# Kernel tuning notes

Hardware: AMD Instinct MI355X
Metric: run time of the kernel (lower is better)

## Reference

```python
import math
import jax, jax.numpy as jnp
import numpy as np

N_HEAD = 16
LORA_SCALE = 16.0 / 8.0  # lora_alpha / r


def lora_linear(x, W, b, A, B):
    # y = x @ W^T + b + scale * (x @ A^T) @ B^T
    base = jnp.einsum('btc,oc->bto', x, W) + b
    low = jnp.einsum('btc,rc->btr', x, A)
    return base + LORA_SCALE * jnp.einsum('btr,or->bto', low, B)


def setup_inputs() -> dict:
    key = jax.random.key(0)
    ks = jax.random.split(key, 8)
    B, T, C = 2, 2048, 1024
    r = 8
    s = 0.02
    return {
        'x': jax.random.normal(ks[0], (B, T, C), jnp.float32),
        'W_attn': jax.random.normal(ks[1], (3 * C, C), jnp.float32) * s,
        'b_attn': jnp.zeros((3 * C,), jnp.float32),
        'A_attn': jax.random.normal(ks[2], (r, C), jnp.float32) * s,
        'B_attn': jax.random.normal(ks[3], (3 * C, r), jnp.float32) * s,
        'W_proj': jax.random.normal(ks[4], (C, C), jnp.float32) * s,
        'b_proj': jnp.zeros((C,), jnp.float32),
        'A_proj': jax.random.normal(ks[5], (r, C), jnp.float32) * s,
        'B_proj': jax.random.normal(ks[6], (C, r), jnp.float32) * s,
    }


def reference(x, W_attn, b_attn, A_attn, B_attn, W_proj, b_proj, A_proj, B_proj):
    B, T, C = x.shape
    H = N_HEAD
    hd = C // H
    qkv = lora_linear(x, W_attn, b_attn, A_attn, B_attn)  # [B,T,3C]
    q, k, v = jnp.split(qkv, 3, axis=2)
    # [B,H,T,hd]
    q = q.reshape(B, T, H, hd).transpose(0, 2, 1, 3)
    k = k.reshape(B, T, H, hd).transpose(0, 2, 1, 3)
    v = v.reshape(B, T, H, hd).transpose(0, 2, 1, 3)
    att = jnp.einsum('bhqd,bhkd->bhqk', q, k) * (1.0 / math.sqrt(hd))
    causal = jnp.tril(jnp.ones((T, T), bool))
    att = jnp.where(causal, att, -jnp.inf)
    att = jax.nn.softmax(att, axis=-1)
    out = jnp.einsum('bhqk,bhkd->bhqd', att, v)
    out = out.transpose(0, 2, 1, 3).reshape(B, T, C)
    return lora_linear(out, W_proj, b_proj, A_proj, B_proj)
```

## Files before the change

kernel.cpp:

```cpp
#include <hip/hip_runtime.h>
#include <hip/hip_bf16.h>
#include <stdint.h>

typedef __bf16 bf16_t;
typedef __bf16 bf16x8 __attribute__((ext_vector_type(8)));
typedef __bf16 bf16x4 __attribute__((ext_vector_type(4)));
typedef __bf16 bf16x2 __attribute__((ext_vector_type(2)));
typedef float f32x4 __attribute__((ext_vector_type(4)));
typedef float f32x16 __attribute__((ext_vector_type(16)));
typedef uint32_t u32;
typedef uint32_t u32x4 __attribute__((ext_vector_type(4)));

typedef __attribute__((address_space(1))) void as1void;
typedef __attribute__((address_space(3))) void as3void;

#define LOG2E 1.44269504088896340736f
#define QSCALE 0.18033688011112042f

__device__ __forceinline__ void gll16(const void* g, void* l) {
  __builtin_amdgcn_global_load_lds((as1void*)g, (as3void*)l, 16, 0, 0);
}

__device__ __forceinline__ u32 pack2(float a, float b) {
  bf16x2 t = {(bf16_t)a, (bf16_t)b};
  return __builtin_bit_cast(u32, t);
}

__global__ void prep_all(const float* __restrict__ W_attn, const float* __restrict__ B_attn,
                         const float* __restrict__ A_attn, const float* __restrict__ W_proj,
                         const float* __restrict__ B_proj, const float* __restrict__ A_proj,
                         const float4* __restrict__ x,
                         bf16_t* __restrict__ WaE, bf16_t* __restrict__ WpE,
                         bf16x4* __restrict__ Xb) {
  int bid = blockIdx.x;
  if (bid < 16384) {
    int idx = bid * 256 + threadIdx.x;
    const float *W, *Bm, *Am;
    bf16_t* dst;
    if (idx < 3145728) {
      W = W_attn; Bm = B_attn; Am = A_attn; dst = WaE;
    } else {
      idx -= 3145728;
      W = W_proj; Bm = B_proj; Am = A_proj; dst = WpE;
    }
    int o = idx >> 10, c = idx & 1023;
    float acc = W[idx];
#pragma unroll
    for (int r = 0; r < 8; ++r)
      acc += 2.0f * Bm[o * 8 + r] * Am[r * 1024 + c];
    dst[idx] = (bf16_t)acc;
  } else {
    int i = (bid - 16384) * 256 + threadIdx.x;
    float4 v = x[i];
    bf16x4 o = {(bf16_t)v.x, (bf16_t)v.y, (bf16_t)v.z, (bf16_t)v.w};
    Xb[i] = o;
  }
}

template <bool QKV>
__global__ __launch_bounds__(256, 3) void gemm_bt(
    const bf16_t* __restrict__ A, const bf16_t* __restrict__ Bt,
    const float* __restrict__ bias,
    bf16_t* __restrict__ Qb, bf16_t* __restrict__ Kb, bf16_t* __restrict__ Vb,
    float* __restrict__ Out) {
  __shared__ bf16_t Als[128][64];
  __shared__ bf16_t Bls[128][64];
  const int m0 = blockIdx.x * 128;
  const int n0 = blockIdx.y * 128;
  const int tid = threadIdx.x;
  const int lane = tid & 63;
  const int w = tid >> 6;
  const int wm = w >> 1, wn = w & 1;
  const int lr = lane & 15, g = lane >> 4;
  const int sw = (lane & 7) << 3;
  const int srow = lane >> 3;
  const int soff = ((lane & 7) ^ srow) * 8;

  f32x4 acc[4][4] = {};

  for (int k0 = 0; k0 < 1024; k0 += 64) {
#pragma unroll
    for (int c = 0; c < 4; ++c) {
      int r = w * 32 + c * 8 + srow;
      gll16(A + (size_t)(m0 + r) * 1024 + k0 + soff, &Als[w * 32 + c * 8][0]);
      gll16(Bt + (size_t)(n0 + r) * 1024 + k0 + soff, &Bls[w * 32 + c * 8][0]);
    }
    __syncthreads();
#pragma unroll
    for (int ks = 0; ks < 2; ++ks) {
      bf16x8 af[4], bfv[4];
#pragma unroll
      for (int i = 0; i < 4; ++i)
        af[i] = *(const bf16x8*)&Als[wm * 64 + i * 16 + lr][(ks * 32 + g * 8) ^ sw];
#pragma unroll
      for (int j = 0; j < 4; ++j)
        bfv[j] = *(const bf16x8*)&Bls[wn * 64 + j * 16 + lr][(ks * 32 + g * 8) ^ sw];
#pragma unroll
      for (int i = 0; i < 4; ++i)
#pragma unroll
        for (int j = 0; j < 4; ++j)
          acc[i][j] = __builtin_amdgcn_mfma_f32_16x16x32_bf16(af[i], bfv[j], acc[i][j], 0, 0, 0);
    }
    __syncthreads();
  }

#pragma unroll
  for (int i = 0; i < 4; ++i) {
#pragma unroll
    for (int j = 0; j < 4; ++j) {
#pragma unroll
      for (int e = 0; e < 4; ++e) {
        int m = m0 + wm * 64 + i * 16 + g * 4 + e;
        int n = n0 + wn * 64 + j * 16 + lr;
        float v = acc[i][j][e] + bias[n];
        if (QKV) {
          int b = m >> 11, t = m & 2047;
          int which = n >> 10, hn = n & 1023;
          int h = hn >> 6, d = hn & 63;
          if (which == 0) v *= QSCALE;
          bf16_t* dst = (which == 0) ? Qb : (which == 1) ? Kb : Vb;
          dst[(((size_t)(b * 16 + h)) * 2048 + t) * 64 + d] = (bf16_t)v;
        } else {
          Out[(size_t)m * 1024 + n] = v;
        }
      }
    }
  }
}

__global__ __launch_bounds__(256, 3) void attn_fwd(
    const bf16_t* __restrict__ Qb, const bf16_t* __restrict__ Kb,
    const bf16_t* __restrict__ Vb, bf16_t* __restrict__ Ob) {
  __shared__ bf16_t Kls[128][64];
  __shared__ bf16_t Vt[2][64][128];

  int id = blockIdx.x;
  int xcd = id & 7, j = id >> 3;
  int lo = j & 31, hi2 = j >> 5;
  int bh = xcd * 4 + (lo & 3);
  int qb = hi2 ? 15 - (lo >> 2) : (lo >> 2);
  int b = bh >> 4, h = bh & 15;

  const int tid = threadIdx.x, lane = tid & 63, w = tid >> 6;
  const int q32 = lane & 31;
  const int hi = lane >> 5;
  const int ksw = (q32 & 7) << 3;
  const int vkey = (q32 >> 2) << 3;
  const bf16_t* Qp = Qb + (size_t)bh * 2048 * 64;
  const bf16_t* Kp = Kb + (size_t)bh * 2048 * 64;
  const bf16_t* Vp = Vb + (size_t)bh * 2048 * 64;

  const int q0 = qb * 128;
  const int qrow = q0 + w * 32 + q32;

  const int kbase = (tid >> 4) * 8;
  const int dbase = (tid & 15) * 4;
  const int wkey = ((tid & 15) & 7) << 3;
  const int ksr = lane >> 3;
  const int kso = ((lane & 7) ^ ksr) * 8;

  bf16x8 qf[4];
#pragma unroll
  for (int ds = 0; ds < 4; ++ds)
    qf[ds] = *(const bf16x8*)(Qp + (size_t)qrow * 64 + ds * 16 + hi * 8);

  float m_run = -3e38f, l_run = 0.f;
  f32x16 o_acc[2] = {};
  const int ktiles = qb + 1;

  {
#pragma unroll
    for (int c = 0; c < 4; ++c) {
      int rb = w * 32 + c * 8;
      gll16(Kp + (size_t)(rb + ksr) * 64 + kso, &Kls[rb][0]);
    }
    uint2 rowv[8];
#pragma unroll
    for (int r = 0; r < 8; ++r)
      rowv[r] = *(const uint2*)(Vp + (size_t)(kbase + r) * 64 + dbase);
#pragma unroll
    for (int dd = 0; dd < 4; ++dd) {
      u32 sel = (dd & 1) ? 0x07060302u : 0x05040100u;
      u32 a0 = (dd >> 1) ? rowv[0].y : rowv[0].x;
      u32 a1 = (dd >> 1) ? rowv[1].y : rowv[1].x;
      u32 a2 = (dd >> 1) ? rowv[2].y : rowv[2].x;
      u32 a3 = (dd >> 1) ? rowv[3].y : rowv[3].x;
      u32 a4 = (dd >> 1) ? rowv[4].y : rowv[4].x;
      u32 a5 = (dd >> 1) ? rowv[5].y : rowv[5].x;
      u32 a6 = (dd >> 1) ? rowv[6].y : rowv[6].x;
      u32 a7 = (dd >> 1) ? rowv[7].y : rowv[7].x;
      int4 val;
      val.x = __builtin_amdgcn_perm(a1, a0, sel);
      val.y = __builtin_amdgcn_perm(a3, a2, sel);
      val.z = __builtin_amdgcn_perm(a5, a4, sel);
      val.w = __builtin_amdgcn_perm(a7, a6, sel);
      *(int4*)&Vt[0][dbase + dd][kbase ^ wkey] = val;
    }
    __syncthreads();
  }

  int cb = 0;
  for (int kt = 0; kt < ktiles; ++kt) {
    const bool lastt = (kt == ktiles - 1);
    const int nfa = lastt ? (w + 1) : 4;
    const int nb = cb ^ 1;

    f32x16 s[4] = {};
    __builtin_amdgcn_s_setprio(1);
#pragma unroll
    for (int fa = 0; fa < 4; ++fa) {
      if (fa < nfa) {
#pragma unroll
        for (int ds = 0; ds < 4; ++ds) {
          bf16x8 kf = *(const bf16x8*)&Kls[fa * 32 + q32][(ds * 16 + hi * 8) ^ ksw];
          s[fa] = __builtin_amdgcn_mfma_f32_32x32x16_bf16(kf, qf[ds], s[fa], 0, 0, 0);
        }
      }
    }
    __builtin_amdgcn_s_setprio(0);
    __syncthreads();

    uint2 rowv[8];
    if (!lastt) {
      const int kn = (kt + 1) * 128;
#pragma unroll
      for (int c = 0; c < 4; ++c) {
        int rb = w * 32 + c * 8;
        gll16(Kp + (size_t)(kn + rb + ksr) * 64 + kso, &Kls[rb][0]);
      }
#pragma unroll
      for (int r = 0; r < 8; ++r)
        rowv[r] = *(const uint2*)(Vp + (size_t)(kn + kbase + r) * 64 + dbase);
    }

    float mloc = -3e38f;
#pragma unroll
    for (int fa = 0; fa < 4; ++fa) {
      if (fa < nfa) {
        if (lastt && fa == w) {
#pragma unroll
          for (int r = 0; r < 16; ++r) {
            int km = (r & 3) + 8 * (r >> 2) + 4 * hi;
            if (km > q32) s[fa][r] = -3e38f;
          }
        }
#pragma unroll
        for (int r = 0; r < 16; ++r) mloc = fmaxf(mloc, s[fa][r]);
      }
    }
    mloc = fmaxf(mloc, __shfl_xor(mloc, 32, 64));
    if (!__all(mloc <= m_run + 8.0f)) {
      float mnew = fmaxf(m_run, mloc);
      float rs = __builtin_amdgcn_exp2f(m_run - mnew);
      m_run = mnew;
      l_run *= rs;
      o_acc[0] *= rs;
      o_acc[1] *= rs;
    }

    if (!lastt) {
#pragma unroll
      for (int dd = 0; dd < 4; ++dd) {
        u32 sel = (dd & 1) ? 0x07060302u : 0x05040100u;
        u32 a0 = (dd >> 1) ? rowv[0].y : rowv[0].x;
        u32 a1 = (dd >> 1) ? rowv[1].y : rowv[1].x;
        u32 a2 = (dd >> 1) ? rowv[2].y : rowv[2].x;
        u32 a3 = (dd >> 1) ? rowv[3].y : rowv[3].x;
        u32 a4 = (dd >> 1) ? rowv[4].y : rowv[4].x;
        u32 a5 = (dd >> 1) ? rowv[5].y : rowv[5].x;
        u32 a6 = (dd >> 1) ? rowv[6].y : rowv[6].x;
        u32 a7 = (dd >> 1) ? rowv[7].y : rowv[7].x;
        int4 val;
        val.x = __builtin_amdgcn_perm(a1, a0, sel);
        val.y = __builtin_amdgcn_perm(a3, a2, sel);
        val.z = __builtin_amdgcn_perm(a5, a4, sel);
        val.w = __builtin_amdgcn_perm(a7, a6, sel);
        *(int4*)&Vt[nb][dbase + dd][kbase ^ wkey] = val;
      }
    }

    float lsum = 0.f;
#pragma unroll
    for (int fa = 0; fa < 4; ++fa) {
      if (fa < nfa) {
        float p[16];
#pragma unroll
        for (int r = 0; r < 16; ++r) {
          p[r] = __builtin_amdgcn_exp2f(s[fa][r] - m_run);
          lsum += p[r];
        }
        u32 x0 = pack2(p[0], p[1]),   x1 = pack2(p[2], p[3]);
        u32 x2 = pack2(p[4], p[5]),   x3 = pack2(p[6], p[7]);
        u32 y0 = pack2(p[8], p[9]),   y1 = pack2(p[10], p[11]);
        u32 y2 = pack2(p[12], p[13]), y3 = pack2(p[14], p[15]);
        u32 z0 = hi ? x0 : x2;
        u32 z1 = hi ? x1 : x3;
        u32 z2 = hi ? y0 : y2;
        u32 z3 = hi ? y1 : y3;
        z0 = (u32)__shfl_xor((int)z0, 32, 64);
        z1 = (u32)__shfl_xor((int)z1, 32, 64);
        z2 = (u32)__shfl_xor((int)z2, 32, 64);
        z3 = (u32)__shfl_xor((int)z3, 32, 64);
        u32x4 pw0 = hi ? (u32x4){z0, z1, x2, x3} : (u32x4){x0, x1, z0, z1};
        u32x4 pw1 = hi ? (u32x4){z2, z3, y2, y3} : (u32x4){y0, y1, z2, z3};
        bf16x8 P0 = __builtin_bit_cast(bf16x8, pw0);
        bf16x8 P1 = __builtin_bit_cast(bf16x8, pw1);
        __builtin_amdgcn_s_setprio(1);
#pragma unroll
        for (int db = 0; db < 2; ++db) {
          int d = db * 32 + q32;
          bf16x8 vf0 = *(const bf16x8*)&Vt[cb][d][(fa * 32 + hi * 8) ^ vkey];
          o_acc[db] = __builtin_amdgcn_mfma_f32_32x32x16_bf16(vf0, P0, o_acc[db], 0, 0, 0);
          bf16x8 vf1 = *(const bf16x8*)&Vt[cb][d][(fa * 32 + 16 + hi * 8) ^ vkey];
          o_acc[db] = __builtin_amdgcn_mfma_f32_32x32x16_bf16(vf1, P1, o_acc[db], 0, 0, 0);
        }
        __builtin_amdgcn_s_setprio(0);
      }
    }
    lsum += __shfl_xor(lsum, 32, 64);
    l_run += lsum;

    __syncthreads();
    cb = nb;
  }

  float inv = 1.0f / l_run;
  bf16_t* obase = Ob + ((size_t)(b * 2048 + qrow)) * 1024 + h * 64;
#pragma unroll
  for (int db = 0; db < 2; ++db) {
#pragma unroll
    for (int rg = 0; rg < 4; ++rg) {
      bf16x4 ov = {(bf16_t)(o_acc[db][rg * 4 + 0] * inv),
                   (bf16_t)(o_acc[db][rg * 4 + 1] * inv),
                   (bf16_t)(o_acc[db][rg * 4 + 2] * inv),
                   (bf16_t)(o_acc[db][rg * 4 + 3] * inv)};
      *(bf16x4*)(obase + db * 32 + rg * 8 + hi * 4) = ov;
    }
  }
}

extern "C" void kernel_launch(void* const* d_in, const int* in_sizes, int n_in,
                              void* d_out, int out_size, void* d_ws, size_t ws_size,
                              hipStream_t stream) {
  const float* x      = (const float*)d_in[0];
  const float* W_attn = (const float*)d_in[1];
  const float* b_attn = (const float*)d_in[2];
  const float* A_attn = (const float*)d_in[3];
  const float* B_attn = (const float*)d_in[4];
  const float* W_proj = (const float*)d_in[5];
  const float* b_proj = (const float*)d_in[6];
  const float* A_proj = (const float*)d_in[7];
  const float* B_proj = (const float*)d_in[8];
  float* out = (float*)d_out;

  char* ws = (char*)d_ws;
  bf16_t* WaE = (bf16_t*)(ws);
  bf16_t* WpE = (bf16_t*)(ws + 6291456);
  bf16_t* Xb  = (bf16_t*)(ws + 8388608);
  bf16_t* Qb  = (bf16_t*)(ws + 16777216);
  bf16_t* Kb  = (bf16_t*)(ws + 25165824);
  bf16_t* Vb  = (bf16_t*)(ws + 33554432);
  bf16_t* Ob  = (bf16_t*)(ws + 41943040);

  prep_all<<<20480, 256, 0, stream>>>(W_attn, B_attn, A_attn, W_proj, B_proj, A_proj,
                                      (const float4*)x, WaE, WpE, (bf16x4*)Xb);

  gemm_bt<true><<<dim3(32, 24), 256, 0, stream>>>(Xb, WaE, b_attn, Qb, Kb, Vb, nullptr);
  attn_fwd<<<512, 256, 0, stream>>>(Qb, Kb, Vb, Ob);
  gemm_bt<false><<<dim3(32, 8), 256, 0, stream>>>(Ob, WpE, b_proj, nullptr, nullptr, nullptr, out);
}
```

Baseline: 118.6 us.

## Split long causal query blocks across two workgroups and merge partial softmax results

Query blocks 8-15 now have their key range split into two halves, each handled by its own workgroup, which writes unnormalized partial outputs plus running max and sum to workspace. A new merge kernel combines them. Blocks are ordered by descending work through a constant table to balance load. K is also double-buffered in LDS so one barrier per tile is dropped, and the V-transpose swizzle changes. The cost is extra partial-output traffic, an extra kernel launch, lower occupancy (launch bounds 2), and reuse of the weight/X workspace regions for partials.

```diff
diff --git a/kernel.cpp b/kernel.cpp
--- a/kernel.cpp
+++ b/kernel.cpp
@@ -14,8 +14,11 @@
 typedef __attribute__((address_space(1))) void as1void;
 typedef __attribute__((address_space(3))) void as3void;
 
-#define LOG2E 1.44269504088896340736f
 #define QSCALE 0.18033688011112042f
+
+__constant__ unsigned char kOrder[24] = {7, 20, 22, 23, 6, 16, 18, 19, 21,
+                                         5, 12, 14, 15, 17, 4, 8, 10, 11, 13,
+                                         3, 9, 2, 1, 0};
 
 __device__ __forceinline__ void gll16(const void* g, void* l) {
   __builtin_amdgcn_global_load_lds((as1void*)g, (as3void*)l, 16, 0, 0);
@@ -128,24 +131,34 @@
   }
 }
 
-__global__ __launch_bounds__(256, 3) void attn_fwd(
+__global__ __launch_bounds__(256, 2) void attn_fwd(
     const bf16_t* __restrict__ Qb, const bf16_t* __restrict__ Kb,
-    const bf16_t* __restrict__ Vb, bf16_t* __restrict__ Ob) {
-  __shared__ bf16_t Kls[128][64];
+    const bf16_t* __restrict__ Vb, bf16_t* __restrict__ Ob,
+    bf16_t* __restrict__ Po, float* __restrict__ Pml) {
+  __shared__ bf16_t Kls[2][128][64];
   __shared__ bf16_t Vt[2][64][128];
 
   int id = blockIdx.x;
-  int xcd = id & 7, j = id >> 3;
-  int lo = j & 31, hi2 = j >> 5;
-  int bh = xcd * 4 + (lo & 3);
-  int qb = hi2 ? 15 - (lo >> 2) : (lo >> 2);
+  int xcd = id & 7, r = id >> 3;
+  int bh = xcd * 4 + (r & 3);
+  int j = kOrder[r >> 2];
+  int qb, kt0, kt1, part;
+  if (j < 8) {
+    qb = j; kt0 = 0; kt1 = qb + 1; part = -1;
+  } else {
+    qb = 8 + ((j - 8) >> 1);
+    part = (j - 8) & 1;
+    int kts = qb + 1, nA = (kts + 1) >> 1;
+    kt0 = part ? nA : 0;
+    kt1 = part ? kts : nA;
+  }
   int b = bh >> 4, h = bh & 15;
 
   const int tid = threadIdx.x, lane = tid & 63, w = tid >> 6;
   const int q32 = lane & 31;
   const int hi = lane >> 5;
   const int ksw = (q32 & 7) << 3;
-  const int vkey = (q32 >> 2) << 3;
+  const int vkey = ((q32 & 7) ^ (q32 >> 2)) << 3;
   const bf16_t* Qp = Qb + (size_t)bh * 2048 * 64;
   const bf16_t* Kp = Kb + (size_t)bh * 2048 * 64;
   const bf16_t* Vp = Vb + (size_t)bh * 2048 * 64;
@@ -155,7 +168,6 @@
 
   const int kbase = (tid >> 4) * 8;
   const int dbase = (tid & 15) * 4;
-  const int wkey = ((tid & 15) & 7) << 3;
   const int ksr = lane >> 3;
   const int kso = ((lane & 7) ^ ksr) * 8;
 
@@ -166,18 +178,18 @@
 
   float m_run = -3e38f, l_run = 0.f;
   f32x16 o_acc[2] = {};
-  const int ktiles = qb + 1;
 
   {
+    const int kp = kt0 * 128;
+    uint2 rowv[8];
+#pragma unroll
+    for (int rr = 0; rr < 8; ++rr)
+      rowv[rr] = *(const uint2*)(Vp + (size_t)(kp + kbase + rr) * 64 + dbase);
 #pragma unroll
     for (int c = 0; c < 4; ++c) {
       int rb = w * 32 + c * 8;
-      gll16(Kp + (size_t)(rb + ksr) * 64 + kso, &Kls[rb][0]);
-    }
-    uint2 rowv[8];
-#pragma unroll
-    for (int r = 0; r < 8; ++r)
-      rowv[r] = *(const uint2*)(Vp + (size_t)(kbase + r) * 64 + dbase);
+      gll16(Kp + (size_t)(kp + rb + ksr) * 64 + kso, &Kls[0][rb][0]);
+    }
 #pragma unroll
     for (int dd = 0; dd < 4; ++dd) {
       u32 sel = (dd & 1) ? 0x07060302u : 0x05040100u;
@@ -194,16 +206,32 @@
       val.y = __builtin_amdgcn_perm(a3, a2, sel);
       val.z = __builtin_amdgcn_perm(a5, a4, sel);
       val.w = __builtin_amdgcn_perm(a7, a6, sel);
-      *(int4*)&Vt[0][dbase + dd][kbase ^ wkey] = val;
+      int d = dbase + dd;
+      int key = ((d & 7) ^ ((d >> 2) & 7)) << 3;
+      *(int4*)&Vt[0][d][kbase ^ key] = val;
     }
     __syncthreads();
   }
 
   int cb = 0;
-  for (int kt = 0; kt < ktiles; ++kt) {
-    const bool lastt = (kt == ktiles - 1);
-    const int nfa = lastt ? (w + 1) : 4;
+  for (int kt = kt0; kt < kt1; ++kt) {
+    const bool haveNext = (kt + 1 < kt1);
+    const bool maskt = (kt == qb);
+    const int nfa = maskt ? (w + 1) : 4;
     const int nb = cb ^ 1;
+
+    uint2 rowv[8];
+    if (haveNext) {
+      const int kn = (kt + 1) * 128;
+#pragma unroll
+      for (int rr = 0; rr < 8; ++rr)
+        rowv[rr] = *(const uint2*)(Vp + (size_t)(kn + kbase + rr) * 64 + dbase);
+#pragma unroll
+      for (int c = 0; c < 4; ++c) {
+        int rb = w * 32 + c * 8;
+        gll16(Kp + (size_t)(kn + rb + ksr) * 64 + kso, &Kls[nb][rb][0]);
+      }
+    }
 
     f32x16 s[4] = {};
     __builtin_amdgcn_s_setprio(1);
@@ -212,40 +240,26 @@
       if (fa < nfa) {
 #pragma unroll
         for (int ds = 0; ds < 4; ++ds) {
-          bf16x8 kf = *(const bf16x8*)&Kls[fa * 32 + q32][(ds * 16 + hi * 8) ^ ksw];
+          bf16x8 kf = *(const bf16x8*)&Kls[cb][fa * 32 + q32][(ds * 16 + hi * 8) ^ ksw];
           s[fa] = __builtin_amdgcn_mfma_f32_32x32x16_bf16(kf, qf[ds], s[fa], 0, 0, 0);
         }
       }
     }
     __builtin_amdgcn_s_setprio(0);
-    __syncthreads();
-
-    uint2 rowv[8];
-    if (!lastt) {
-      const int kn = (kt + 1) * 128;
-#pragma unroll
-      for (int c = 0; c < 4; ++c) {
-        int rb = w * 32 + c * 8;
-        gll16(Kp + (size_t)(kn + rb + ksr) * 64 + kso, &Kls[rb][0]);
-      }
-#pragma unroll
-      for (int r = 0; r < 8; ++r)
-        rowv[r] = *(const uint2*)(Vp + (size_t)(kn + kbase + r) * 64 + dbase);
-    }
 
     float mloc = -3e38f;
 #pragma unroll
     for (int fa = 0; fa < 4; ++fa) {
       if (fa < nfa) {
-        if (lastt && fa == w) {
-#pragma unroll
-          for (int r = 0; r < 16; ++r) {
-            int km = (r & 3) + 8 * (r >> 2) + 4 * hi;
-            if (km > q32) s[fa][r] = -3e38f;
+        if (maskt && fa == w) {
+#pragma unroll
+          for (int rr = 0; rr < 16; ++rr) {
+            int km = (rr & 3) + 8 * (rr >> 2) + 4 * hi;
+            if (km > q32) s[fa][rr] = -3e38f;
           }
         }
 #pragma unroll
-        for (int r = 0; r < 16; ++r) mloc = fmaxf(mloc, s[fa][r]);
+        for (int rr = 0; rr < 16; ++rr) mloc = fmaxf(mloc, s[fa][rr]);
       }
     }
     mloc = fmaxf(mloc, __shfl_xor(mloc, 32, 64));
@@ -258,7 +272,7 @@
       o_acc[1] *= rs;
     }
 
-    if (!lastt) {
+    if (haveNext) {
 #pragma unroll
       for (int dd = 0; dd < 4; ++dd) {
         u32 sel = (dd & 1) ? 0x07060302u : 0x05040100u;
@@ -275,7 +289,9 @@
         val.y = __builtin_amdgcn_perm(a3, a2, sel);
         val.z = __builtin_amdgcn_perm(a5, a4, sel);
         val.w = __builtin_amdgcn_perm(a7, a6, sel);
-        *(int4*)&Vt[nb][dbase + dd][kbase ^ wkey] = val;
+        int d = dbase + dd;
+        int key = ((d & 7) ^ ((d >> 2) & 7)) << 3;
+        *(int4*)&Vt[nb][d][kbase ^ key] = val;
       }
     }
 
@@ -285,9 +301,9 @@
       if (fa < nfa) {
         float p[16];
 #pragma unroll
-        for (int r = 0; r < 16; ++r) {
-          p[r] = __builtin_amdgcn_exp2f(s[fa][r] - m_run);
-          lsum += p[r];
+        for (int rr = 0; rr < 16; ++rr) {
+          p[rr] = __builtin_amdgcn_exp2f(s[fa][rr] - m_run);
+          lsum += p[rr];
         }
         u32 x0 = pack2(p[0], p[1]),   x1 = pack2(p[2], p[3]);
         u32 x2 = pack2(p[4], p[5]),   x3 = pack2(p[6], p[7]);
@@ -324,18 +340,72 @@
     cb = nb;
   }
 
-  float inv = 1.0f / l_run;
-  bf16_t* obase = Ob + ((size_t)(b * 2048 + qrow)) * 1024 + h * 64;
-#pragma unroll
-  for (int db = 0; db < 2; ++db) {
-#pragma unroll
-    for (int rg = 0; rg < 4; ++rg) {
-      bf16x4 ov = {(bf16_t)(o_acc[db][rg * 4 + 0] * inv),
-                   (bf16_t)(o_acc[db][rg * 4 + 1] * inv),
-                   (bf16_t)(o_acc[db][rg * 4 + 2] * inv),
-                   (bf16_t)(o_acc[db][rg * 4 + 3] * inv)};
-      *(bf16x4*)(obase + db * 32 + rg * 8 + hi * 4) = ov;
-    }
+  if (part < 0) {
+    float inv = 1.0f / l_run;
+    bf16_t* obase = Ob + ((size_t)(b * 2048 + qrow)) * 1024 + h * 64;
+#pragma unroll
+    for (int db = 0; db < 2; ++db) {
+#pragma unroll
+      for (int rg = 0; rg < 4; ++rg) {
+        bf16x4 ov = {(bf16_t)(o_acc[db][rg * 4 + 0] * inv),
+                     (bf16_t)(o_acc[db][rg * 4 + 1] * inv),
+                     (bf16_t)(o_acc[db][rg * 4 + 2] * inv),
+                     (bf16_t)(o_acc[db][rg * 4 + 3] * inv)};
+        *(bf16x4*)(obase + db * 32 + rg * 8 + hi * 4) = ov;
+      }
+    }
+  } else {
+    int sidx = bh * 16 + (qb - 8) * 2 + part;
+    int prow = w * 32 + q32;
+    bf16_t* po = Po + (size_t)sidx * 8192 + prow * 64;
+#pragma unroll
+    for (int db = 0; db < 2; ++db) {
+#pragma unroll
+      for (int rg = 0; rg < 4; ++rg) {
+        bf16x4 ov = {(bf16_t)o_acc[db][rg * 4 + 0], (bf16_t)o_acc[db][rg * 4 + 1],
+                     (bf16_t)o_acc[db][rg * 4 + 2], (bf16_t)o_acc[db][rg * 4 + 3]};
+        *(bf16x4*)(po + db * 32 + rg * 8 + hi * 4) = ov;
+      }
+    }
+    if (hi == 0) {
+      Pml[sidx * 256 + prow * 2] = m_run;
+      Pml[sidx * 256 + prow * 2 + 1] = l_run;
+    }
+  }
+}
+
+__global__ __launch_bounds__(256) void attn_merge(
+    const bf16_t* __restrict__ Po, const float* __restrict__ Pml,
+    bf16_t* __restrict__ Ob) {
+  int blk = blockIdx.x;
+  int bh = blk >> 3, qb8 = blk & 7;
+  int qb = 8 + qb8;
+  int b = bh >> 4, h = bh & 15;
+  int sA = bh * 16 + qb8 * 2, sB = sA + 1;
+  int t = threadIdx.x;
+  int row = t >> 1, c0 = (t & 1) * 32;
+
+  float mA = Pml[sA * 256 + row * 2], lA = Pml[sA * 256 + row * 2 + 1];
+  float mB = Pml[sB * 256 + row * 2], lB = Pml[sB * 256 + row * 2 + 1];
+  float m = fmaxf(mA, mB);
+  float wA = __builtin_amdgcn_exp2f(mA - m);
+  float wB = __builtin_amdgcn_exp2f(mB - m);
+  float inv = 1.0f / (lA * wA + lB * wB);
+  wA *= inv;
+  wB *= inv;
+
+  const bf16_t* pa = Po + (size_t)sA * 8192 + row * 64 + c0;
+  const bf16_t* pb = Po + (size_t)sB * 8192 + row * 64 + c0;
+  bf16_t* ob = Ob + ((size_t)(b * 2048 + qb * 128 + row)) * 1024 + h * 64 + c0;
+#pragma unroll
+  for (int u = 0; u < 4; ++u) {
+    bf16x8 a = *(const bf16x8*)(pa + u * 8);
+    bf16x8 c = *(const bf16x8*)(pb + u * 8);
+    bf16x8 o;
+#pragma unroll
+    for (int i = 0; i < 8; ++i)
+      o[i] = (bf16_t)((float)a[i] * wA + (float)c[i] * wB);
+    *(bf16x8*)(ob + u * 8) = o;
   }
 }
 
@@ -361,11 +431,14 @@
   bf16_t* Kb  = (bf16_t*)(ws + 25165824);
   bf16_t* Vb  = (bf16_t*)(ws + 33554432);
   bf16_t* Ob  = (bf16_t*)(ws + 41943040);
+  float*  Pml = (float*)(ws);
+  bf16_t* Po  = (bf16_t*)(ws + 8388608);
 
   prep_all<<<20480, 256, 0, stream>>>(W_attn, B_attn, A_attn, W_proj, B_proj, A_proj,
                                       (const float4*)x, WaE, WpE, (bf16x4*)Xb);
 
   gemm_bt<true><<<dim3(32, 24), 256, 0, stream>>>(Xb, WaE, b_attn, Qb, Kb, Vb, nullptr);
-  attn_fwd<<<512, 256, 0, stream>>>(Qb, Kb, Vb, Ob);
+  attn_fwd<<<768, 256, 0, stream>>>(Qb, Kb, Vb, Ob, Po, Pml);
+  attn_merge<<<256, 256, 0, stream>>>(Po, Pml, Ob);
   gemm_bt<false><<<dim3(32, 8), 256, 0, stream>>>(Ob, WpE, b_proj, nullptr, nullptr, nullptr, out);
 }
```

New measurement: 113.0 us. -4.7%, faster.
